# Kernel tuning notes

Measured on AMD Instinct MI355X. Metric: run time of the kernel, lower is better.

## Reference

```python
import jax, jax.numpy as jnp
import numpy as np

KEYS = ["A1", "B2", "E1", "E2", "E3", "E4", "E5"]
DIMS = [1, 1, 2, 2, 2, 2, 2]  # irrep dimensions for D12 point group
H = 8  # num_heads


def setup_inputs() -> dict:
    key = jax.random.key(0)
    ks = jax.random.split(key, 11)
    B, S, M = 8, 1024, 64  # batch, seq_len, multiplicity per key
    inp = {}
    for i, (name, d) in enumerate(zip(KEYS, DIMS)):
        inp[f"x_{name}"] = jax.random.normal(ks[i], (B, S, d, M), dtype=jnp.float32)
    for j, wn in enumerate(["Wq", "Wk", "Wv", "Wo"]):
        # per-key nn.Linear weights [out_mult, in_mult], stacked over the 7 keys
        inp[wn] = jax.random.normal(ks[7 + j], (7, M, M), dtype=jnp.float32) / np.float32(np.sqrt(M))
    return inp


def _split_heads(v):
    # [B,S,d,m] -> [B,H,S,d*mk]
    B, S, d, m = v.shape
    mk = m // H
    return v.reshape(B, S, d, H, mk).transpose(0, 3, 1, 2, 4).reshape(B, H, S, d * mk)


def _combine_heads(v, d):
    # [B,H,S,d*mk] -> [B,S,d,H*mk]
    B, _, S, dmk = v.shape
    mk = dmk // d
    return v.reshape(B, H, S, d, mk).transpose(0, 2, 3, 1, 4).reshape(B, S, d, H * mk)


def _forward(xs, Wq, Wk, Wv, Wo):
    # per-key bias-free linears on the multiplicity (last) axis; nn.Linear does x @ W.T
    qs = [_split_heads(jnp.einsum('bsdi,oi->bsdo', x, Wq[i])) for i, x in enumerate(xs)]
    kks = [_split_heads(jnp.einsum('bsdi,oi->bsdo', x, Wk[i])) for i, x in enumerate(xs)]
    vs = [_split_heads(jnp.einsum('bsdi,oi->bsdo', x, Wv[i])) for i, x in enumerate(xs)]
    Q = jnp.concatenate(qs, axis=-1)  # [B,H,S,D], D = sum d_k*mk = 96
    K = jnp.concatenate(kks, axis=-1)
    scale = np.float32(1.0 / np.sqrt(Q.shape[-1]))
    probs = jax.nn.softmax(jnp.einsum('bhqd,bhkd->bhqk', Q, K) * scale, axis=-1)
    outs = []
    for i, (v, d) in enumerate(zip(vs, DIMS)):
        o = jnp.einsum('bhqk,bhkd->bhqd', probs, v)  # shared softmax over per-key V branches
        o = _combine_heads(o, d)  # [B,S,d,M]
        outs.append(jnp.einsum('bsdi,oi->bsdo', o, Wo[i]))
    # concatenate the 7 per-key outputs along the irrep-dimension axis: [B,S,12,M]
    return jnp.concatenate(outs, axis=2)


def reference(x_A1, x_B2, x_E1, x_E2, x_E3, x_E4, x_E5, Wq, Wk, Wv, Wo):
    xs = [x_A1, x_B2, x_E1, x_E2, x_E3, x_E4, x_E5]
    return _forward(xs, Wq, Wk, Wv, Wo)
```

## Files before the change

### kernel.cpp

```cpp
#include <hip/hip_runtime.h>
#include <stdint.h>

typedef __attribute__((ext_vector_type(8))) short bf16x8;
typedef __attribute__((ext_vector_type(4))) float f32x4;
typedef unsigned short ushort_t;

#define NE 6291456

__device__ __forceinline__ unsigned short f2bf(float f){
  union { float f; unsigned u; } c; c.f = f;
  unsigned u = c.u;
  u = u + 0x7FFFu + ((u >> 16) & 1u);
  return (unsigned short)(u >> 16);
}

__device__ __forceinline__ bf16x8 cvt8(const float* p){
  const float4 a = ((const float4*)p)[0];
  const float4 b = ((const float4*)p)[1];
  bf16x8 r;
  r[0]=(short)f2bf(a.x); r[1]=(short)f2bf(a.y); r[2]=(short)f2bf(a.z); r[3]=(short)f2bf(a.w);
  r[4]=(short)f2bf(b.x); r[5]=(short)f2bf(b.y); r[6]=(short)f2bf(b.z); r[7]=(short)f2bf(b.w);
  return r;
}

__device__ __forceinline__ uint32_t pk2bf(float a, float b){
  uint32_t r;
  asm("v_cvt_pk_bf16_f32 %0, %1, %2" : "=v"(r) : "v"(a), "v"(b));
  return r;
}

__device__ __forceinline__ float exp2x(float x){
  float r;
  asm("v_exp_f32 %0, %1" : "=v"(r) : "v"(x));
  return r;
}

__device__ __forceinline__ void rr_decode(int rr, int& i, int& dx, int& d){
  if (rr < 2){ i = rr; dx = 0; d = 1; }
  else { i = 2 + ((rr-2)>>1); dx = (rr-2)&1; d = 2; }
}

__global__ __launch_bounds__(256) void wconv(
    const float* __restrict__ Wq, const float* __restrict__ Wk,
    const float* __restrict__ Wv, const float* __restrict__ Wo,
    ushort_t* __restrict__ out)
{
  const int a = blockIdx.y;
  const float* src = (a==0)?Wq:(a==1)?Wk:(a==2)?Wv:Wo;
  const float sc = (a==0) ? 0.14724743479535623f : 1.0f;
  const int i = (blockIdx.x*256 + threadIdx.x)*8;
  float4 v0 = *(const float4*)(src+i);
  float4 v1 = *(const float4*)(src+i+4);
  uint4 o;
  o.x = pk2bf(v0.x*sc, v0.y*sc);
  o.y = pk2bf(v0.z*sc, v0.w*sc);
  o.z = pk2bf(v1.x*sc, v1.y*sc);
  o.w = pk2bf(v1.z*sc, v1.w*sc);
  *(uint4*)(out + (size_t)a*28672 + i) = o;
}

__global__ __launch_bounds__(256) void qkv_proj(
    const float* __restrict__ xA1, const float* __restrict__ xB2,
    const float* __restrict__ xE1, const float* __restrict__ xE2,
    const float* __restrict__ xE3, const float* __restrict__ xE4,
    const float* __restrict__ xE5,
    const ushort_t* __restrict__ Wb4,
    ushort_t* __restrict__ Qg, ushort_t* __restrict__ KVg)
{
  __shared__ short Cl[64*72];

  const int tile = blockIdx.x;
  const int rr = tile >> 7, rt = tile & 127;
  int i, dx, d; rr_decode(rr, i, dx, d);
  const float* xp = (i==0)?xA1:(i==1)?xB2:(i==2)?xE1:(i==3)?xE2:(i==4)?xE3:(i==5)?xE4:xE5;

  const int lane = threadIdx.x & 63;
  const int w    = threadIdx.x >> 6;
  const int lo = lane & 15, hi = lane >> 4;
  const int b8 = (rt >> 4) * 8;
  const int tile64 = rt & 15;

  bf16x8 afr[2];
  {
    const int R = rt*64 + w*16 + lo;
    const float* rp = xp + (size_t)(R*d + dx) * 64;
    afr[0] = cvt8(rp + 8*hi);
    afr[1] = cvt8(rp + 32 + 8*hi);
  }

  {
    const ushort_t* Wb = Wb4 + (size_t)i * 4096;
    #pragma unroll
    for (int ot = 0; ot < 4; ++ot){
      f32x4 acc = {0.f,0.f,0.f,0.f};
      #pragma unroll
      for (int c = 0; c < 2; ++c){
        bf16x8 bfr = *(const bf16x8*)(Wb + (size_t)(lo + 16*ot) * 64 + 32*c + 8*hi);
        acc = __builtin_amdgcn_mfma_f32_16x16x32_bf16(bfr, afr[c], acc, 0, 0, 0);
      }
      uint2 o2;
      o2.x = pk2bf(acc[0], acc[1]);
      o2.y = pk2bf(acc[2], acc[3]);
      int hh = 2*ot + (hi>>1);
      size_t a = (size_t)((b8 + hh)*16 + tile64)*6144
               + (size_t)((w*3 + (rr>>2))*64 + (rr&3)*16 + lo)*8 + 4*(hi&1);
      *(uint2*)(Qg + a) = o2;
    }
  }

  {
    const ushort_t* Wb = Wb4 + (size_t)28672 + (size_t)i * 4096;
    #pragma unroll
    for (int ot = 0; ot < 4; ++ot){
      f32x4 acc = {0.f,0.f,0.f,0.f};
      #pragma unroll
      for (int c = 0; c < 2; ++c){
        bf16x8 bfr = *(const bf16x8*)(Wb + (size_t)(lo + 16*ot) * 64 + 32*c + 8*hi);
        acc = __builtin_amdgcn_mfma_f32_16x16x32_bf16(bfr, afr[c], acc, 0, 0, 0);
      }
      uint2 o2;
      o2.x = pk2bf(acc[0], acc[1]);
      o2.y = pk2bf(acc[2], acc[3]);
      int hh = 2*ot + (hi>>1);
      size_t a = (size_t)((b8 + hh)*32 + tile64*2 + (w>>1))*6144
               + (size_t)(((w&1)*3 + (rr>>2))*64 + (rr&3)*16 + lo)*8 + 4*(hi&1);
      *(uint2*)(KVg + a) = o2;
    }
  }

  {
    const ushort_t* Wb = Wb4 + (size_t)2*28672 + (size_t)i * 4096;
    #pragma unroll
    for (int ot = 0; ot < 4; ++ot){
      f32x4 acc = {0.f,0.f,0.f,0.f};
      #pragma unroll
      for (int c = 0; c < 2; ++c){
        bf16x8 bfr = *(const bf16x8*)(Wb + (size_t)(lo + 16*ot) * 64 + 32*c + 8*hi);
        acc = __builtin_amdgcn_mfma_f32_16x16x32_bf16(afr[c], bfr, acc, 0, 0, 0);
      }
      #pragma unroll
      for (int r = 0; r < 4; ++r)
        Cl[(w*16 + hi*4 + r)*72 + lo + 16*ot] = (short)f2bf(acc[r]);
    }
    __syncthreads();
    #pragma unroll
    for (int cc = 0; cc < 2; ++cc){
      int c2 = threadIdx.x + cc*256;
      int mm = c2 & 7, hh = (c2>>3)&7, sblk = c2>>6;
      int a5 = sblk>>2, slot = sblk&3;
      short tmp[8];
      #pragma unroll
      for (int jj = 0; jj < 8; ++jj){
        int s_j = a5*32 + (jj>>2)*16 + slot*4 + (jj&3);
        tmp[jj] = Cl[s_j*72 + hh*8 + mm];
      }
      int fh = rr>>1, fl = (rr&1)*8 + mm;
      size_t a = (size_t)((b8 + hh)*32 + tile64*2 + a5)*6144 + 3072
               + (size_t)(fh*64 + slot*16 + fl)*8;
      *(bf16x8*)(KVg + a) = *(const bf16x8*)tmp;
    }
  }
}

__global__ __launch_bounds__(256, 2) void attn(
    const ushort_t* __restrict__ Qg,
    const ushort_t* __restrict__ KVg,
    ushort_t* __restrict__ Oc)
{
  __shared__ __align__(16) float facc[2*6*4*64*4];
  __shared__ float Lx[2][4][64];

  const int bid = blockIdx.x;
  const int bh = (bid & 7)*8 + ((bid >> 3) & 7);
  const int qt = bid >> 6;
  const int tid = threadIdx.x;
  const int w = tid >> 6, lane = tid & 63;
  const int wq = w & 1, wk = w >> 1;
  const int lo = lane & 15, hi = lane >> 4;
  const size_t qbase  = (size_t)bh * 16 * 6144;
  const size_t kvbase = (size_t)bh * 32 * 6144;

  bf16x8 qf[4][3];
  {
    const ushort_t* qb = Qg + qbase + (size_t)(2*qt + wq)*6144;
    #pragma unroll
    for (int g = 0; g < 4; ++g)
      #pragma unroll
      for (int c = 0; c < 3; ++c)
        qf[g][c] = *(const bf16x8*)(qb + ((g*3 + c)*64 + lane)*8);
  }

  f32x4 acc[6][4];
  #pragma unroll
  for (int ft = 0; ft < 6; ++ft)
    #pragma unroll
    for (int g = 0; g < 4; ++g) acc[ft][g] = (f32x4){0,0,0,0};
  float lr[4] = {0.f, 0.f, 0.f, 0.f};

  for (int j = 0; j < 16; ++j){
    const ushort_t* kvt = KVg + kvbase + (size_t)(2*j + wk)*6144;

    f32x4 st[4][2];
    __builtin_amdgcn_s_setprio(1);
    #pragma unroll
    for (int kvb = 0; kvb < 2; ++kvb){
      bf16x8 kf[3];
      #pragma unroll
      for (int c = 0; c < 3; ++c)
        kf[c] = *(const bf16x8*)(kvt + ((kvb*3 + c)*64 + lane)*8);
      #pragma unroll
      for (int g = 0; g < 4; ++g){
        f32x4 s = {0.f,0.f,0.f,0.f};
        #pragma unroll
        for (int c = 0; c < 3; ++c)
          s = __builtin_amdgcn_mfma_f32_16x16x32_bf16(kf[c], qf[g][c], s, 0, 0, 0);
        st[g][kvb] = s;
      }
    }
    __builtin_amdgcn_s_setprio(0);

    bf16x8 pb[4];
    #pragma unroll
    for (int g = 0; g < 4; ++g){
      #pragma unroll
      for (int kvb = 0; kvb < 2; ++kvb)
        #pragma unroll
        for (int r = 0; r < 4; ++r){ st[g][kvb][r] = exp2x(st[g][kvb][r]); lr[g] += st[g][kvb][r]; }
      union { uint32_t u[4]; bf16x8 v; } pu;
      pu.u[0] = pk2bf(st[g][0][0], st[g][0][1]);
      pu.u[1] = pk2bf(st[g][0][2], st[g][0][3]);
      pu.u[2] = pk2bf(st[g][1][0], st[g][1][1]);
      pu.u[3] = pk2bf(st[g][1][2], st[g][1][3]);
      pb[g] = pu.v;
    }

    __builtin_amdgcn_s_setprio(1);
    #pragma unroll
    for (int ft = 0; ft < 6; ++ft){
      bf16x8 va = *(const bf16x8*)(kvt + 3072 + (ft*64 + lane)*8);
      #pragma unroll
      for (int g = 0; g < 4; ++g)
        acc[ft][g] = __builtin_amdgcn_mfma_f32_16x16x32_bf16(va, pb[g], acc[ft][g], 0, 0, 0);
    }
    __builtin_amdgcn_s_setprio(0);
  }

  #pragma unroll
  for (int g = 0; g < 4; ++g){
    lr[g] += __shfl_xor(lr[g], 16);
    lr[g] += __shfl_xor(lr[g], 32);
  }

  if (wk == 1){
    #pragma unroll
    for (int ft = 0; ft < 6; ++ft)
      #pragma unroll
      for (int g = 0; g < 4; ++g)
        *(f32x4*)&facc[(((wq*6 + ft)*4 + g)*64 + lane)*4] = acc[ft][g];
    #pragma unroll
    for (int g = 0; g < 4; ++g) Lx[wq][g][lane] = lr[g];
  }
  __syncthreads();
  if (wk == 0){
    float rl[4];
    #pragma unroll
    for (int g = 0; g < 4; ++g) rl[g] = 1.f / (lr[g] + Lx[wq][g][lane]);
    #pragma unroll
    for (int ft = 0; ft < 6; ++ft){
      #pragma unroll
      for (int g = 0; g < 4; ++g){
        f32x4 o = acc[ft][g] + *(const f32x4*)&facc[(((wq*6 + ft)*4 + g)*64 + lane)*4];
        uint2 ou;
        ou.x = pk2bf(o[0]*rl[g], o[1]*rl[g]);
        ou.y = pk2bf(o[2]*rl[g], o[3]*rl[g]);
        int q = qt*128 + wq*64 + g*16 + lo;
        size_t ad = ((size_t)(bh*24 + ft*4 + hi)*1024 + q)*4;
        *(uint2*)(Oc + ad) = ou;
      }
    }
  }
}

__global__ __launch_bounds__(256) void out_proj(
    const ushort_t* __restrict__ Oc,
    const ushort_t* __restrict__ Wb4,
    float* __restrict__ out)
{
  const int tile = blockIdx.x;
  const int rr = tile >> 7, rt = tile & 127;
  int i, dx, d; rr_decode(rr, i, dx, d); (void)dx; (void)d;

  const int lane = threadIdx.x & 63;
  const int w    = threadIdx.x >> 6;
  const int lo = lane & 15, hi = lane >> 4;

  bf16x8 afr[2];
  {
    const int R = rt*64 + w*16 + lo;
    const int b = R >> 10, s = R & 1023;
    union { uint2 u2[2]; bf16x8 v; } a0, a1;
    #pragma unroll
    for (int jj = 0; jj < 2; ++jj){
      a0.u2[jj] = *(const uint2*)(Oc + ((size_t)((b*8 + hi)*24 + 2*rr + jj)*1024 + s)*4);
      a1.u2[jj] = *(const uint2*)(Oc + ((size_t)((b*8 + 4 + hi)*24 + 2*rr + jj)*1024 + s)*4);
    }
    afr[0] = a0.v;
    afr[1] = a1.v;
  }

  const ushort_t* Wb = Wb4 + (size_t)3*28672 + (size_t)i * 4096;
  #pragma unroll
  for (int ot = 0; ot < 4; ++ot){
    f32x4 acc = {0.f,0.f,0.f,0.f};
    #pragma unroll
    for (int c = 0; c < 2; ++c){
      bf16x8 bfr = *(const bf16x8*)(Wb + (size_t)(lo + 16*ot) * 64 + 32*c + 8*hi);
      acc = __builtin_amdgcn_mfma_f32_16x16x32_bf16(afr[c], bfr, acc, 0, 0, 0);
    }
    #pragma unroll
    for (int r = 0; r < 4; ++r){
      int bs = rt*64 + w*16 + hi*4 + r;
      out[(size_t)(bs*12 + rr)*64 + lo + 16*ot] = acc[r];
    }
  }
}

extern "C" void kernel_launch(void* const* d_in, const int* in_sizes, int n_in,
                              void* d_out, int out_size, void* d_ws, size_t ws_size,
                              hipStream_t stream)
{
  const float* xA1 = (const float*)d_in[0];
  const float* xB2 = (const float*)d_in[1];
  const float* xE1 = (const float*)d_in[2];
  const float* xE2 = (const float*)d_in[3];
  const float* xE3 = (const float*)d_in[4];
  const float* xE4 = (const float*)d_in[5];
  const float* xE5 = (const float*)d_in[6];
  const float* Wq  = (const float*)d_in[7];
  const float* Wk  = (const float*)d_in[8];
  const float* Wv  = (const float*)d_in[9];
  const float* Wo  = (const float*)d_in[10];

  ushort_t* Qg  = (ushort_t*)d_ws;
  ushort_t* KVg = Qg + NE;
  ushort_t* Oc  = KVg + (size_t)2*NE;
  ushort_t* Wb4 = Oc + NE;

  wconv<<<dim3(14,4), dim3(256), 0, stream>>>(Wq, Wk, Wv, Wo, Wb4);
  qkv_proj<<<dim3(1536), dim3(256), 0, stream>>>(xA1,xB2,xE1,xE2,xE3,xE4,xE5,
                                                 Wb4, Qg, KVg);
  attn<<<dim3(512), dim3(256), 0, stream>>>(Qg, KVg, Oc);
  out_proj<<<dim3(1536), dim3(256), 0, stream>>>(Oc, Wb4, (float*)d_out);
}
```

Baseline: 81.46 us.

## Double-buffer K tiles in LDS via async loads and prefetch V into registers

K tiles for the attention loop are now staged into a double-buffered LDS array with global_load_lds, shared by the two query waves that use the same KV tile. V fragments for the next iteration are prefetched into registers. A block-wide barrier now ends each iteration. The aim is to hide global-load latency behind the MFMA work and to stop each wave re-reading K from global memory. In exchange it uses more LDS and registers, which may lower occupancy, and adds a sync every iteration.

```diff
diff --git a/kernel.cpp b/kernel.cpp
--- a/kernel.cpp
+++ b/kernel.cpp
@@ -33,6 +33,12 @@
   float r;
   asm("v_exp_f32 %0, %1" : "=v"(r) : "v"(x));
   return r;
+}
+
+__device__ __forceinline__ void gll16(const ushort_t* g, short* l){
+  __builtin_amdgcn_global_load_lds(
+      (const __attribute__((address_space(1))) unsigned int*)g,
+      (__attribute__((address_space(3))) unsigned int*)l, 16, 0, 0);
 }
 
 __device__ __forceinline__ void rr_decode(int rr, int& i, int& dx, int& d){
@@ -167,6 +173,7 @@
     const ushort_t* __restrict__ KVg,
     ushort_t* __restrict__ Oc)
 {
+  __shared__ __align__(16) short Kl[2][2][3072];
   __shared__ __align__(16) float facc[2*6*4*64*4];
   __shared__ float Lx[2][4][64];
 
@@ -197,8 +204,37 @@
     for (int g = 0; g < 4; ++g) acc[ft][g] = (f32x4){0,0,0,0};
   float lr[4] = {0.f, 0.f, 0.f, 0.f};
 
+#define STAGEK(jj, bb) do { \
+    const ushort_t* kg_ = KVg + kvbase + (size_t)(2*(jj)+wk)*6144 + wq*1536 + lane*8; \
+    short* l_ = &Kl[wk][bb][wq*1536 + lane*8]; \
+    gll16(kg_, l_); gll16(kg_ + 512, l_ + 512); gll16(kg_ + 1024, l_ + 1024); \
+  } while(0)
+
+  bf16x8 vnext[6];
+  {
+    const ushort_t* vg = KVg + kvbase + (size_t)wk*6144 + 3072;
+    #pragma unroll
+    for (int ft = 0; ft < 6; ++ft)
+      vnext[ft] = *(const bf16x8*)(vg + (ft*64 + lane)*8);
+  }
+
+  STAGEK(0, 0);
+  __syncthreads();
+
   for (int j = 0; j < 16; ++j){
-    const ushort_t* kvt = KVg + kvbase + (size_t)(2*j + wk)*6144;
+    if (j < 15) STAGEK(j+1, (j+1)&1);
+
+    bf16x8 vcur[6];
+    #pragma unroll
+    for (int ft = 0; ft < 6; ++ft) vcur[ft] = vnext[ft];
+    if (j < 15){
+      const ushort_t* vg = KVg + kvbase + (size_t)(2*(j+1)+wk)*6144 + 3072;
+      #pragma unroll
+      for (int ft = 0; ft < 6; ++ft)
+        vnext[ft] = *(const bf16x8*)(vg + (ft*64 + lane)*8);
+    }
+
+    const short* kb = &Kl[wk][j&1][0];
 
     f32x4 st[4][2];
     __builtin_amdgcn_s_setprio(1);
@@ -207,7 +243,7 @@
       bf16x8 kf[3];
       #pragma unroll
       for (int c = 0; c < 3; ++c)
-        kf[c] = *(const bf16x8*)(kvt + ((kvb*3 + c)*64 + lane)*8);
+        kf[c] = *(const bf16x8*)&kb[((kvb*3 + c)*64 + lane)*8];
       #pragma unroll
       for (int g = 0; g < 4; ++g){
         f32x4 s = {0.f,0.f,0.f,0.f};
@@ -237,13 +273,15 @@
     __builtin_amdgcn_s_setprio(1);
     #pragma unroll
     for (int ft = 0; ft < 6; ++ft){
-      bf16x8 va = *(const bf16x8*)(kvt + 3072 + (ft*64 + lane)*8);
       #pragma unroll
       for (int g = 0; g < 4; ++g)
-        acc[ft][g] = __builtin_amdgcn_mfma_f32_16x16x32_bf16(va, pb[g], acc[ft][g], 0, 0, 0);
+        acc[ft][g] = __builtin_amdgcn_mfma_f32_16x16x32_bf16(vcur[ft], pb[g], acc[ft][g], 0, 0, 0);
     }
     __builtin_amdgcn_s_setprio(0);
-  }
+
+    __syncthreads();
+  }
+#undef STAGEK
 
   #pragma unroll
   for (int g = 0; g < 4; ++g){
```

Measured after the change: 72.37 us. -11.2%, faster.
